# Optimization experiments

Measured on AMD Instinct MI355X. Metric: run time of the kernel, lower is better.

## Reference

```python
import jax, jax.numpy as jnp
import numpy as np

B, C, H, W = 16, 128, 64, 64
L, ND = 512, 256
GROUPS = 32
EPS = 1e-6


def setup_inputs() -> dict:
    key = jax.random.key(0)
    ks = jax.random.split(key, 8)
    return {
        "x": jax.random.normal(ks[0], (B, C, H, W), dtype=jnp.float32),
        "nd": jax.random.normal(ks[1], (B, L, ND), dtype=jnp.float32),
        "gn_gamma": jnp.ones((C,), dtype=jnp.float32),
        "gn_beta": jnp.zeros((C,), dtype=jnp.float32),
        "q_w": jax.random.normal(ks[2], (C, C), dtype=jnp.float32) * 0.02,
        "q_b": jax.random.normal(ks[3], (C,), dtype=jnp.float32) * 0.02,
        "nd_w": jax.random.normal(ks[4], (C, ND), dtype=jnp.float32) * 0.02,
        "nd_b": jax.random.normal(ks[5], (C,), dtype=jnp.float32) * 0.02,
        "proj_w": jax.random.normal(ks[6], (C, C), dtype=jnp.float32) * 0.02,
        "proj_b": jax.random.normal(ks[7], (C,), dtype=jnp.float32) * 0.02,
    }


def _group_norm(x, gamma, beta):
    b, c, h, w = x.shape
    xr = x.reshape(b, GROUPS, c // GROUPS, h, w)
    mean = xr.mean(axis=(2, 3, 4), keepdims=True)
    var = xr.var(axis=(2, 3, 4), keepdims=True)
    xn = ((xr - mean) * jax.lax.rsqrt(var + EPS)).reshape(b, c, h, w)
    return xn * gamma[None, :, None, None] + beta[None, :, None, None]


def reference(x, nd, gn_gamma, gn_beta, q_w, q_b, nd_w, nd_b, proj_w, proj_b):
    b, c, h, w = x.shape
    hn = _group_norm(x, gn_gamma, gn_beta)
    # 1x1 conv query -> [b, hw, c]
    q = jnp.einsum('bchw,oc->bhwo', hn, q_w).reshape(b, h * w, c) + q_b
    # silu + linear projection of conditioning; k and v use identical projection/input
    kv = jax.nn.silu(nd) @ nd_w.T + nd_b  # [b, L, c]
    # attention: [b, hw, L]
    logits = jnp.einsum('bnc,blc->bnl', q, kv) * (c ** -0.5)
    attn = jax.nn.softmax(logits, axis=2)
    # weighted sum of v -> [b, c, hw] -> [b, c, h, w]
    out = jnp.einsum('blc,bnl->bcn', kv, attn).reshape(b, c, h, w)
    # 1x1 conv projection
    out = jnp.einsum('bchw,oc->bohw', out, proj_w) + proj_b[None, :, None, None]
    return x + out
```

## Files before the change

kernel.cpp:

```cpp
#include <hip/hip_runtime.h>
#include <math.h>

constexpr int kB = 16, kC = 128, kHW = 4096, kL = 512, kND = 256, kG = 32;
constexpr float kEps = 1e-6f;
constexpr float kScale = 0.08838834764831845f;

typedef short sv8 __attribute__((ext_vector_type(8)));
typedef int   iv4 __attribute__((ext_vector_type(4)));
typedef float f32x16 __attribute__((ext_vector_type(16)));

static __device__ __forceinline__ unsigned short f2bf(float f) {
    unsigned int u = __builtin_bit_cast(unsigned int, f);
    u += 0x7fffu + ((u >> 16) & 1u);
    return (unsigned short)(u >> 16);
}
static __device__ __forceinline__ float bf2f(unsigned short s) {
    unsigned int u = ((unsigned int)s) << 16;
    return __builtin_bit_cast(float, u);
}
static __device__ __forceinline__ unsigned int pack2(float a, float b) {
    return (unsigned int)f2bf(a) | ((unsigned int)f2bf(b) << 16);
}

#define GLOAD_LDS16(gp, lp)                                                     \
    __builtin_amdgcn_global_load_lds(                                           \
        (const __attribute__((address_space(1))) void*)(gp),                    \
        (__attribute__((address_space(3))) void*)(lp), 16, 0, 0)

__global__ __launch_bounds__(256) void prep_all_k(
    const float* __restrict__ x, const float* __restrict__ nd,
    const float* __restrict__ nd_w, const float* __restrict__ nd_b,
    const float* __restrict__ proj_w,
    float* __restrict__ stats, unsigned short* __restrict__ kv_bf,
    unsigned short* __restrict__ kvT_bf, unsigned short* __restrict__ pwb)
{
    __shared__ float s_lds[8][256];
    __shared__ float w_lds[128][68];
    __shared__ float t_lds[8][129];
    __shared__ float red8[8];
    const int bid = blockIdx.x;
    const int tid = threadIdx.x;

    if (bid < 512) {
        const float4* p4 = (const float4*)(x + (size_t)bid * 4 * kHW);
        float s = 0.f, ss = 0.f;
        for (int i = tid; i < 4096; i += 256) {
            float4 v = p4[i];
            s  += (v.x + v.y) + (v.z + v.w);
            ss += (v.x * v.x + v.y * v.y) + (v.z * v.z + v.w * v.w);
        }
#pragma unroll
        for (int off = 1; off < 64; off <<= 1) {
            s  += __shfl_xor(s, off, 64);
            ss += __shfl_xor(ss, off, 64);
        }
        int wid = tid >> 6;
        if ((tid & 63) == 0) { red8[wid] = s; red8[wid + 4] = ss; }
        __syncthreads();
        if (tid == 0) {
            float S  = (red8[0] + red8[1]) + (red8[2] + red8[3]);
            float SS = (red8[4] + red8[5]) + (red8[6] + red8[7]);
            float mean = S * (1.f / 16384.f);
            float var  = SS * (1.f / 16384.f) - mean * mean;
            stats[bid * 2]     = mean;
            stats[bid * 2 + 1] = rsqrtf(var + kEps);
        }
        return;
    }
    if (bid >= 1536) {
        int i = ((bid - 1536) * 256 + tid) * 4;
        float4 v = *(const float4*)(proj_w + i);
        pwb[i + 0] = f2bf(v.x); pwb[i + 1] = f2bf(v.y);
        pwb[i + 2] = f2bf(v.z); pwb[i + 3] = f2bf(v.w);
        return;
    }
    {
        int idx0 = bid - 512;
        int b = idx0 >> 6;
        int l0 = (idx0 & 63) * 8;
        const float4* ndp = (const float4*)(nd + ((size_t)b * kL + l0) * kND);
#pragma unroll
        for (int r = 0; r < 2; r++) {
            int idx = tid + r * 256;
            int row = idx >> 6;
            int c4 = idx & 63;
            float4 v = ndp[row * 64 + c4];
            v.x = v.x / (1.f + __expf(-v.x));
            v.y = v.y / (1.f + __expf(-v.y));
            v.z = v.z / (1.f + __expf(-v.z));
            v.w = v.w / (1.f + __expf(-v.w));
            *(float4*)&s_lds[row][c4 * 4] = v;
        }
        float acc[4] = {0.f, 0.f, 0.f, 0.f};
        int lr = tid >> 5;
        int oq = tid & 31;
        for (int d0 = 0; d0 < kND; d0 += 64) {
            __syncthreads();
#pragma unroll
            for (int r = 0; r < 8; r++) {
                int idx = tid + r * 256;
                int row = idx >> 4;
                int c4 = idx & 15;
                float4 v = ((const float4*)(nd_w + (size_t)row * kND + d0))[c4];
                *(float4*)&w_lds[row][c4 * 4] = v;
            }
            __syncthreads();
            for (int dd = 0; dd < 64; dd += 4) {
                float4 sv = *(const float4*)&s_lds[lr][d0 + dd];
#pragma unroll
                for (int j = 0; j < 4; j++) {
                    float4 wv = *(const float4*)&w_lds[oq + 32 * j][dd];
                    acc[j] += sv.x * wv.x + sv.y * wv.y + sv.z * wv.z + sv.w * wv.w;
                }
            }
        }
#pragma unroll
        for (int j = 0; j < 4; j++) {
            int o = oq + 32 * j;
            float vout = acc[j] + nd_b[o];
            kv_bf[((size_t)b * kL + l0 + lr) * kC + o] = f2bf(vout);
            t_lds[lr][o] = vout;
        }
        __syncthreads();
        int o = tid >> 1, lh = (tid & 1) * 4;
        unsigned long long pk = 0;
#pragma unroll
        for (int i = 0; i < 4; i++)
            pk |= (unsigned long long)f2bf(t_lds[lh + i][o]) << (16 * i);
        *(unsigned long long*)(kvT_bf + ((size_t)b * kC + o) * kL + l0 + lh) = pk;
    }
}

__global__ __launch_bounds__(256, 2) void attn_k(
    const float* __restrict__ x,
    const float* __restrict__ stats,
    const float* __restrict__ gamma,
    const float* __restrict__ beta,
    const float* __restrict__ q_w,
    const float* __restrict__ q_b,
    const unsigned short* __restrict__ kvb,
    const unsigned short* __restrict__ kvtb,
    const unsigned short* __restrict__ pwb,
    const float* __restrict__ proj_b,
    float* __restrict__ out)
{
    __shared__ __align__(16) char smem[36864];

    const int flat = blockIdx.y * gridDim.x + blockIdx.x;
    const int b  = ((flat & 7) << 1) | ((flat >> 3) & 1);
    const int n0 = (flat >> 4) * 128;
    const int tid = threadIdx.x;
    const int wave = tid >> 6;
    const int lane = tid & 63;
    const int lrow = lane & 31;
    const int hi = lane >> 5;
    const int swzA = (lrow & 15) << 4;
    const int swzT = ((lrow >> 1) & 3) << 4;

    unsigned short* qw = (unsigned short*)smem;
    float* gtab = (float*)(smem + 34816);

    if (tid < 128) {
        float mean = stats[(b * kG + (tid >> 2)) * 2];
        float rstd = stats[(b * kG + (tid >> 2)) * 2 + 1];
        float ga = gamma[tid] * rstd;
        gtab[tid] = ga;
        gtab[128 + tid] = beta[tid] - mean * ga;
        gtab[256 + tid] = q_b[tid];
    }
#pragma unroll
    for (int r = 0; r < 16; r++) {
        int idx = tid + r * 256;
        int row = idx >> 5, c4 = idx & 31;
        float4 v = ((const float4*)q_w)[idx];
        unsigned int lo = (unsigned int)f2bf(v.x) | ((unsigned int)f2bf(v.y) << 16);
        unsigned int h2 = (unsigned int)f2bf(v.z) | ((unsigned int)f2bf(v.w) << 16);
        *(uint2*)&qw[row * 136 + c4 * 4] = make_uint2(lo, h2);
    }
    __syncthreads();

    sv8 hn[8];
    {
        const float* xp = x + (size_t)b * kC * kHW + n0 + wave * 32 + lrow;
#pragma unroll
        for (int kc = 0; kc < 8; kc++) {
            int cb = kc * 16 + hi * 8;
            sv8 a;
#pragma unroll
            for (int j = 0; j < 8; j++) {
                float ga = gtab[cb + j], be = gtab[128 + cb + j];
                a[j] = (short)f2bf(xp[(size_t)(cb + j) * kHW] * ga + be);
            }
            hn[kc] = a;
        }
    }
    f32x16 dq[4];
#pragma unroll
    for (int ot = 0; ot < 4; ot++)
#pragma unroll
        for (int r = 0; r < 16; r++) dq[ot][r] = 0.f;
#pragma unroll
    for (int ot = 0; ot < 4; ot++) {
        const unsigned short* arow = qw + (ot * 32 + lrow) * 136 + hi * 8;
#pragma unroll
        for (int kc = 0; kc < 8; kc++)
            dq[ot] = __builtin_amdgcn_mfma_f32_32x32x16_bf16(
                         *(const sv8*)(arow + kc * 16), hn[kc], dq[ot], 0, 0, 0);
    }
    sv8 qa[8];
#pragma unroll
    for (int ot = 0; ot < 4; ot++) {
        unsigned int pk[4], pk2[4];
#pragma unroll
        for (int g = 0; g < 4; g++) {
            int ob = ot * 32 + 8 * g + 4 * hi;
            float v0 = (dq[ot][4 * g + 0] + gtab[256 + ob + 0]) * kScale;
            float v1 = (dq[ot][4 * g + 1] + gtab[256 + ob + 1]) * kScale;
            float v2 = (dq[ot][4 * g + 2] + gtab[256 + ob + 2]) * kScale;
            float v3 = (dq[ot][4 * g + 3] + gtab[256 + ob + 3]) * kScale;
            pk[g]  = pack2(v0, v1);
            pk2[g] = pack2(v2, v3);
        }
#pragma unroll
        for (int kk = 0; kk < 2; kk++) {
            unsigned int a_lo = pk[kk * 2],  a_hi = pk[kk * 2 + 1];
            unsigned int b_lo = pk2[kk * 2], b_hi = pk2[kk * 2 + 1];
            unsigned int own_a = hi ? a_hi : a_lo;
            unsigned int own_b = hi ? b_hi : b_lo;
            unsigned int rcv_a = (unsigned int)__shfl_xor((int)(hi ? a_lo : a_hi), 32, 64);
            unsigned int rcv_b = (unsigned int)__shfl_xor((int)(hi ? b_lo : b_hi), 32, 64);
            iv4 w;
            w[0] = (int)(hi ? rcv_a : own_a);
            w[1] = (int)(hi ? rcv_b : own_b);
            w[2] = (int)(hi ? own_a : rcv_a);
            w[3] = (int)(hi ? own_b : rcv_b);
            qa[2 * ot + kk] = __builtin_bit_cast(sv8, w);
        }
    }
    __syncthreads();

    f32x16 oacc[4];
#pragma unroll
    for (int ct = 0; ct < 4; ct++)
#pragma unroll
        for (int r = 0; r < 16; r++) oacc[ct][r] = 0.f;
    float rsumv = 0.f;

    const unsigned short* kvB  = kvb  + (size_t)b * kL * kC;
    const unsigned short* kvtB = kvtb + (size_t)b * kC * kL;

#define STAGE_TILE(tt) do {                                                     \
        int l0s = (tt) << 5;                                                    \
        char* dA = smem + (((tt) & 1) * 8192);                                  \
        char* dT = smem + 16384 + (((tt) & 1) * 8192);                          \
        _Pragma("unroll")                                                       \
        for (int i = 0; i < 2; i++) {                                           \
            int l = i * 16 + wave * 4 + (lane >> 4);                            \
            int ch = lane & 15;                                                 \
            const unsigned short* gs =                                          \
                kvB + (size_t)(l0s + l) * kC + ((ch ^ (l & 15)) * 8);           \
            GLOAD_LDS16(gs, dA + (i * 256 + wave * 64) * 16);                   \
        }                                                                       \
        _Pragma("unroll")                                                       \
        for (int i = 0; i < 2; i++) {                                           \
            int c = i * 64 + wave * 16 + (lane >> 2);                           \
            int ch = lane & 3;                                                  \
            const unsigned short* gs =                                          \
                kvtB + (size_t)c * kL + l0s + ((ch ^ ((c >> 1) & 3)) * 8);      \
            GLOAD_LDS16(gs, dT + (i * 256 + wave * 64) * 16);                   \
        }                                                                       \
    } while (0)

    STAGE_TILE(0);
    __syncthreads();

    for (int t = 0; t < 16; t++) {
        const char* bufA = smem + (t & 1) * 8192;
        const char* bufT = smem + 16384 + (t & 1) * 8192;
        if (t < 15) STAGE_TILE(t + 1);

        f32x16 s;
#pragma unroll
        for (int r = 0; r < 16; r++) s[r] = 0.f;
        {
            const char* arow = bufA + lrow * 256;
            __builtin_amdgcn_s_setprio(1);
#pragma unroll
            for (int kc = 0; kc < 8; kc++)
                s = __builtin_amdgcn_mfma_f32_32x32x16_bf16(
                        *(const sv8*)(arow + ((kc * 32 + hi * 16) ^ swzA)),
                        qa[kc], s, 0, 0, 0);
            __builtin_amdgcn_s_setprio(0);
        }
        float p[16];
#pragma unroll
        for (int r = 0; r < 16; r++) {
            p[r] = __expf(s[r]);
            rsumv += p[r];
        }
        unsigned int pk[4], pk2[4];
#pragma unroll
        for (int g = 0; g < 4; g++) {
            pk[g]  = pack2(p[4 * g + 0], p[4 * g + 1]);
            pk2[g] = pack2(p[4 * g + 2], p[4 * g + 3]);
        }
        sv8 pv[2];
#pragma unroll
        for (int kk = 0; kk < 2; kk++) {
            unsigned int a_lo = pk[kk * 2],  a_hi = pk[kk * 2 + 1];
            unsigned int b_lo = pk2[kk * 2], b_hi = pk2[kk * 2 + 1];
            unsigned int own_a = hi ? a_hi : a_lo;
            unsigned int own_b = hi ? b_hi : b_lo;
            unsigned int rcv_a = (unsigned int)__shfl_xor((int)(hi ? a_lo : a_hi), 32, 64);
            unsigned int rcv_b = (unsigned int)__shfl_xor((int)(hi ? b_lo : b_hi), 32, 64);
            iv4 w;
            w[0] = (int)(hi ? rcv_a : own_a);
            w[1] = (int)(hi ? rcv_b : own_b);
            w[2] = (int)(hi ? own_a : rcv_a);
            w[3] = (int)(hi ? own_b : rcv_b);
            pv[kk] = __builtin_bit_cast(sv8, w);
        }
        __builtin_amdgcn_s_setprio(1);
#pragma unroll
        for (int ct = 0; ct < 4; ct++) {
            const char* rowp = bufT + (ct * 32 + lrow) * 64;
#pragma unroll
            for (int kk = 0; kk < 2; kk++)
                oacc[ct] = __builtin_amdgcn_mfma_f32_32x32x16_bf16(
                               pv[kk],
                               *(const sv8*)(rowp + ((kk * 32 + hi * 16) ^ swzT)),
                               oacc[ct], 0, 0, 0);
        }
        __builtin_amdgcn_s_setprio(0);

        __syncthreads();
    }

    float total = rsumv + __shfl_xor(rsumv, 32, 64);
    float* rs = (float*)(smem + 36352) + wave * 32;
    rs[lrow] = 1.0f / total;
    float rinv[16];
#pragma unroll
    for (int r = 0; r < 16; r++)
        rinv[r] = rs[(r & 3) + 8 * (r >> 2) + 4 * hi];

    unsigned short* o_lds = (unsigned short*)smem;
    __syncthreads();
#pragma unroll
    for (int ct = 0; ct < 4; ct++)
#pragma unroll
        for (int r = 0; r < 16; r++) {
            int n = wave * 32 + (r & 3) + 8 * (r >> 2) + 4 * hi;
            o_lds[n * 136 + ct * 32 + lrow] = f2bf(oacc[ct][r] * rinv[r]);
        }
    sv8 oa[8];
    {
        const unsigned short* orow = o_lds + (wave * 32 + lrow) * 136 + hi * 8;
#pragma unroll
        for (int kc = 0; kc < 8; kc++) oa[kc] = *(const sv8*)(orow + kc * 16);
    }
    f32x16 dacc[4];
#pragma unroll
    for (int ot = 0; ot < 4; ot++)
#pragma unroll
        for (int r = 0; r < 16; r++) dacc[ot][r] = 0.f;
#pragma unroll
    for (int ot = 0; ot < 4; ot++) {
        const unsigned short* brow = pwb + (ot * 32 + lrow) * kC + hi * 8;
#pragma unroll
        for (int kc = 0; kc < 8; kc++)
            dacc[ot] = __builtin_amdgcn_mfma_f32_32x32x16_bf16(
                           oa[kc], *(const sv8*)(brow + kc * 16), dacc[ot], 0, 0, 0);
    }
#pragma unroll
    for (int ot = 0; ot < 4; ot++)
#pragma unroll
        for (int r = 0; r < 16; r++) {
            int n = wave * 32 + (r & 3) + 8 * (r >> 2) + 4 * hi;
            o_lds[n * 136 + ot * 32 + lrow] = f2bf(dacc[ot][r]);
        }
    __syncthreads();
#pragma unroll 4
    for (int it = 0; it < 64; it++) {
        int idx = it * 256 + tid;
        int o = idx >> 7, n = idx & 127;
        size_t gi = ((size_t)b * kC + o) * kHW + n0 + n;
        out[gi] = bf2f(o_lds[n * 136 + o]) + proj_b[o] + x[gi];
    }
#undef STAGE_TILE
}

extern "C" void kernel_launch(void* const* d_in, const int* in_sizes, int n_in,
                              void* d_out, int out_size, void* d_ws, size_t ws_size,
                              hipStream_t stream) {
    const float* x      = (const float*)d_in[0];
    const float* nd     = (const float*)d_in[1];
    const float* gamma  = (const float*)d_in[2];
    const float* beta   = (const float*)d_in[3];
    const float* q_w    = (const float*)d_in[4];
    const float* q_b    = (const float*)d_in[5];
    const float* nd_w   = (const float*)d_in[6];
    const float* nd_b   = (const float*)d_in[7];
    const float* proj_w = (const float*)d_in[8];
    const float* proj_b = (const float*)d_in[9];
    float* out = (float*)d_out;

    float* stats           = (float*)d_ws;
    unsigned short* pwb    = (unsigned short*)(stats + 1024);
    unsigned short* kv_bf  = pwb + 16384;
    unsigned short* kvT_bf = kv_bf + (size_t)kB * kL * kC;

    prep_all_k<<<dim3(1552), dim3(256), 0, stream>>>(
        x, nd, nd_w, nd_b, proj_w, stats, kv_bf, kvT_bf, pwb);
    attn_k<<<dim3(kHW / 128, kB), dim3(256), 0, stream>>>(
        x, stats, gamma, beta, q_w, q_b, kv_bf, kvT_bf, pwb, proj_b, out);
}
```

Baseline: 81.16 us.

## Overlap first KV tile staging with query projection prologue

Issues the first K/V tile async load before the query-projection prologue, so the staging overlaps the GroupNorm and Q GEMM work. The prologue is restructured: all 64 x values are loaded into registers up front, and the q_w weight is staged in two halves through a separate LDS region so the attention buffers stay untouched. LDS grows from 36 KB to 51 KB per block, which may still allow two blocks per CU. The trade-offs are higher register pressure from 64 extra live floats and an added barrier.

```diff
diff --git a/kernel.cpp b/kernel.cpp
--- a/kernel.cpp
+++ b/kernel.cpp
@@ -144,7 +144,7 @@
     const float* __restrict__ proj_b,
     float* __restrict__ out)
 {
-    __shared__ __align__(16) char smem[36864];
+    __shared__ __align__(16) char smem[52224];
 
     const int flat = blockIdx.y * gridDim.x + blockIdx.x;
     const int b  = ((flat & 7) << 1) | ((flat >> 3) & 1);
@@ -157,94 +157,8 @@
     const int swzA = (lrow & 15) << 4;
     const int swzT = ((lrow >> 1) & 3) << 4;
 
-    unsigned short* qw = (unsigned short*)smem;
-    float* gtab = (float*)(smem + 34816);
-
-    if (tid < 128) {
-        float mean = stats[(b * kG + (tid >> 2)) * 2];
-        float rstd = stats[(b * kG + (tid >> 2)) * 2 + 1];
-        float ga = gamma[tid] * rstd;
-        gtab[tid] = ga;
-        gtab[128 + tid] = beta[tid] - mean * ga;
-        gtab[256 + tid] = q_b[tid];
-    }
-#pragma unroll
-    for (int r = 0; r < 16; r++) {
-        int idx = tid + r * 256;
-        int row = idx >> 5, c4 = idx & 31;
-        float4 v = ((const float4*)q_w)[idx];
-        unsigned int lo = (unsigned int)f2bf(v.x) | ((unsigned int)f2bf(v.y) << 16);
-        unsigned int h2 = (unsigned int)f2bf(v.z) | ((unsigned int)f2bf(v.w) << 16);
-        *(uint2*)&qw[row * 136 + c4 * 4] = make_uint2(lo, h2);
-    }
-    __syncthreads();
-
-    sv8 hn[8];
-    {
-        const float* xp = x + (size_t)b * kC * kHW + n0 + wave * 32 + lrow;
-#pragma unroll
-        for (int kc = 0; kc < 8; kc++) {
-            int cb = kc * 16 + hi * 8;
-            sv8 a;
-#pragma unroll
-            for (int j = 0; j < 8; j++) {
-                float ga = gtab[cb + j], be = gtab[128 + cb + j];
-                a[j] = (short)f2bf(xp[(size_t)(cb + j) * kHW] * ga + be);
-            }
-            hn[kc] = a;
-        }
-    }
-    f32x16 dq[4];
-#pragma unroll
-    for (int ot = 0; ot < 4; ot++)
-#pragma unroll
-        for (int r = 0; r < 16; r++) dq[ot][r] = 0.f;
-#pragma unroll
-    for (int ot = 0; ot < 4; ot++) {
-        const unsigned short* arow = qw + (ot * 32 + lrow) * 136 + hi * 8;
-#pragma unroll
-        for (int kc = 0; kc < 8; kc++)
-            dq[ot] = __builtin_amdgcn_mfma_f32_32x32x16_bf16(
-                         *(const sv8*)(arow + kc * 16), hn[kc], dq[ot], 0, 0, 0);
-    }
-    sv8 qa[8];
-#pragma unroll
-    for (int ot = 0; ot < 4; ot++) {
-        unsigned int pk[4], pk2[4];
-#pragma unroll
-        for (int g = 0; g < 4; g++) {
-            int ob = ot * 32 + 8 * g + 4 * hi;
-            float v0 = (dq[ot][4 * g + 0] + gtab[256 + ob + 0]) * kScale;
-            float v1 = (dq[ot][4 * g + 1] + gtab[256 + ob + 1]) * kScale;
-            float v2 = (dq[ot][4 * g + 2] + gtab[256 + ob + 2]) * kScale;
-            float v3 = (dq[ot][4 * g + 3] + gtab[256 + ob + 3]) * kScale;
-            pk[g]  = pack2(v0, v1);
-            pk2[g] = pack2(v2, v3);
-        }
-#pragma unroll
-        for (int kk = 0; kk < 2; kk++) {
-            unsigned int a_lo = pk[kk * 2],  a_hi = pk[kk * 2 + 1];
-            unsigned int b_lo = pk2[kk * 2], b_hi = pk2[kk * 2 + 1];
-            unsigned int own_a = hi ? a_hi : a_lo;
-            unsigned int own_b = hi ? b_hi : b_lo;
-            unsigned int rcv_a = (unsigned int)__shfl_xor((int)(hi ? a_lo : a_hi), 32, 64);
-            unsigned int rcv_b = (unsigned int)__shfl_xor((int)(hi ? b_lo : b_hi), 32, 64);
-            iv4 w;
-            w[0] = (int)(hi ? rcv_a : own_a);
-            w[1] = (int)(hi ? rcv_b : own_b);
-            w[2] = (int)(hi ? own_a : rcv_a);
-            w[3] = (int)(hi ? own_b : rcv_b);
-            qa[2 * ot + kk] = __builtin_bit_cast(sv8, w);
-        }
-    }
-    __syncthreads();
-
-    f32x16 oacc[4];
-#pragma unroll
-    for (int ct = 0; ct < 4; ct++)
-#pragma unroll
-        for (int r = 0; r < 16; r++) oacc[ct][r] = 0.f;
-    float rsumv = 0.f;
+    unsigned short* qw = (unsigned short*)(smem + 32768);
+    float* gtab = (float*)(smem + 50176);
 
     const unsigned short* kvB  = kvb  + (size_t)b * kL * kC;
     const unsigned short* kvtB = kvtb + (size_t)b * kC * kL;
@@ -272,7 +186,130 @@
     } while (0)
 
     STAGE_TILE(0);
+
+    if (tid < 128) {
+        float mean = stats[(b * kG + (tid >> 2)) * 2];
+        float rstd = stats[(b * kG + (tid >> 2)) * 2 + 1];
+        float ga = gamma[tid] * rstd;
+        gtab[tid] = ga;
+        gtab[128 + tid] = beta[tid] - mean * ga;
+        gtab[256 + tid] = q_b[tid];
+    }
+    float xv[64];
+    {
+        const float* xp = x + (size_t)b * kC * kHW + n0 + wave * 32 + lrow;
+#pragma unroll
+        for (int c = 0; c < 64; c++) {
+            int ch = (c >> 3) * 16 + hi * 8 + (c & 7);
+            xv[c] = xp[(size_t)ch * kHW];
+        }
+    }
+#pragma unroll
+    for (int r = 0; r < 8; r++) {
+        int idx = tid + r * 256;
+        int row = idx >> 5, c4 = idx & 31;
+        float4 v = ((const float4*)q_w)[row * 32 + c4];
+        unsigned int lo = (unsigned int)f2bf(v.x) | ((unsigned int)f2bf(v.y) << 16);
+        unsigned int h2 = (unsigned int)f2bf(v.z) | ((unsigned int)f2bf(v.w) << 16);
+        *(uint2*)&qw[row * 136 + c4 * 4] = make_uint2(lo, h2);
+    }
     __syncthreads();
+
+    float4 cv[8];
+#pragma unroll
+    for (int r = 0; r < 8; r++) {
+        int idx = tid + r * 256;
+        int row = idx >> 5, c4 = idx & 31;
+        cv[r] = ((const float4*)q_w)[(64 + row) * 32 + c4];
+    }
+    sv8 hn[8];
+#pragma unroll
+    for (int kc = 0; kc < 8; kc++) {
+        int cb = kc * 16 + hi * 8;
+        float4 g0 = *(const float4*)&gtab[cb];
+        float4 g1 = *(const float4*)&gtab[cb + 4];
+        float4 e0 = *(const float4*)&gtab[128 + cb];
+        float4 e1 = *(const float4*)&gtab[128 + cb + 4];
+        sv8 a;
+        a[0] = (short)f2bf(xv[kc * 8 + 0] * g0.x + e0.x);
+        a[1] = (short)f2bf(xv[kc * 8 + 1] * g0.y + e0.y);
+        a[2] = (short)f2bf(xv[kc * 8 + 2] * g0.z + e0.z);
+        a[3] = (short)f2bf(xv[kc * 8 + 3] * g0.w + e0.w);
+        a[4] = (short)f2bf(xv[kc * 8 + 4] * g1.x + e1.x);
+        a[5] = (short)f2bf(xv[kc * 8 + 5] * g1.y + e1.y);
+        a[6] = (short)f2bf(xv[kc * 8 + 6] * g1.z + e1.z);
+        a[7] = (short)f2bf(xv[kc * 8 + 7] * g1.w + e1.w);
+        hn[kc] = a;
+    }
+    f32x16 dq[4];
+#pragma unroll
+    for (int ot = 0; ot < 4; ot++)
+#pragma unroll
+        for (int r = 0; r < 16; r++) dq[ot][r] = 0.f;
+#pragma unroll
+    for (int ot = 0; ot < 2; ot++) {
+        const unsigned short* arow = qw + (ot * 32 + lrow) * 136 + hi * 8;
+#pragma unroll
+        for (int kc = 0; kc < 8; kc++)
+            dq[ot] = __builtin_amdgcn_mfma_f32_32x32x16_bf16(
+                         *(const sv8*)(arow + kc * 16), hn[kc], dq[ot], 0, 0, 0);
+    }
+    __syncthreads();
+#pragma unroll
+    for (int r = 0; r < 8; r++) {
+        int idx = tid + r * 256;
+        int row = idx >> 5, c4 = idx & 31;
+        float4 v = cv[r];
+        unsigned int lo = (unsigned int)f2bf(v.x) | ((unsigned int)f2bf(v.y) << 16);
+        unsigned int h2 = (unsigned int)f2bf(v.z) | ((unsigned int)f2bf(v.w) << 16);
+        *(uint2*)&qw[row * 136 + c4 * 4] = make_uint2(lo, h2);
+    }
+    __syncthreads();
+#pragma unroll
+    for (int ot = 2; ot < 4; ot++) {
+        const unsigned short* arow = qw + ((ot - 2) * 32 + lrow) * 136 + hi * 8;
+#pragma unroll
+        for (int kc = 0; kc < 8; kc++)
+            dq[ot] = __builtin_amdgcn_mfma_f32_32x32x16_bf16(
+                         *(const sv8*)(arow + kc * 16), hn[kc], dq[ot], 0, 0, 0);
+    }
+    sv8 qa[8];
+#pragma unroll
+    for (int ot = 0; ot < 4; ot++) {
+        unsigned int pk[4], pk2[4];
+#pragma unroll
+        for (int g = 0; g < 4; g++) {
+            int ob = ot * 32 + 8 * g + 4 * hi;
+            float v0 = (dq[ot][4 * g + 0] + gtab[256 + ob + 0]) * kScale;
+            float v1 = (dq[ot][4 * g + 1] + gtab[256 + ob + 1]) * kScale;
+            float v2 = (dq[ot][4 * g + 2] + gtab[256 + ob + 2]) * kScale;
+            float v3 = (dq[ot][4 * g + 3] + gtab[256 + ob + 3]) * kScale;
+            pk[g]  = pack2(v0, v1);
+            pk2[g] = pack2(v2, v3);
+        }
+#pragma unroll
+        for (int kk = 0; kk < 2; kk++) {
+            unsigned int a_lo = pk[kk * 2],  a_hi = pk[kk * 2 + 1];
+            unsigned int b_lo = pk2[kk * 2], b_hi = pk2[kk * 2 + 1];
+            unsigned int own_a = hi ? a_hi : a_lo;
+            unsigned int own_b = hi ? b_hi : b_lo;
+            unsigned int rcv_a = (unsigned int)__shfl_xor((int)(hi ? a_lo : a_hi), 32, 64);
+            unsigned int rcv_b = (unsigned int)__shfl_xor((int)(hi ? b_lo : b_hi), 32, 64);
+            iv4 w;
+            w[0] = (int)(hi ? rcv_a : own_a);
+            w[1] = (int)(hi ? rcv_b : own_b);
+            w[2] = (int)(hi ? own_a : rcv_a);
+            w[3] = (int)(hi ? own_b : rcv_b);
+            qa[2 * ot + kk] = __builtin_bit_cast(sv8, w);
+        }
+    }
+
+    f32x16 oacc[4];
+#pragma unroll
+    for (int ct = 0; ct < 4; ct++)
+#pragma unroll
+        for (int r = 0; r < 16; r++) oacc[ct][r] = 0.f;
+    float rsumv = 0.f;
 
     for (int t = 0; t < 16; t++) {
         const char* bufA = smem + (t & 1) * 8192;
@@ -337,7 +374,7 @@
     }
 
     float total = rsumv + __shfl_xor(rsumv, 32, 64);
-    float* rs = (float*)(smem + 36352) + wave * 32;
+    float* rs = (float*)(smem + 51712) + wave * 32;
     rs[lrow] = 1.0f / total;
     float rinv[16];
 #pragma unroll
```

After: 80.62 us. About the same (-0.7%).

## Split query projection into separate kernel writing bf16 Q to workspace

Applied to the files above, without the earlier changes.

Moves the GroupNorm-apply and 1x1 query convolution out of the attention kernel into a new qproj_k kernel. That kernel stages x and bf16 weights in swizzled LDS with coalesced float4 loads and writes scaled bf16 Q to workspace. The attention kernel then just loads its Q fragments directly, which replaces the strided per-channel x reads and shuffles and cuts its LDS use. The cost is an extra kernel launch plus a write and re-read of Q (16x4096x128 bf16) through global memory.

```diff
diff --git a/kernel.cpp b/kernel.cpp
--- a/kernel.cpp
+++ b/kernel.cpp
@@ -131,20 +131,111 @@
     }
 }
 
+__global__ __launch_bounds__(256) void qproj_k(
+    const float* __restrict__ x, const float* __restrict__ stats,
+    const float* __restrict__ gamma, const float* __restrict__ beta,
+    const float* __restrict__ q_w, const float* __restrict__ q_b,
+    unsigned short* __restrict__ q_bf)
+{
+    __shared__ __align__(16) char smem[44032];
+    const int b = blockIdx.y;
+    const int n0 = blockIdx.x * 128;
+    const int tid = threadIdx.x;
+    const int wave = tid >> 6, lane = tid & 63;
+    const int lrow = lane & 31, hi = lane >> 5;
+
+    unsigned short* hn = (unsigned short*)(smem + 32768);
+    float* gab = (float*)(smem + 43008);
+
+    if (tid < 128) {
+        float mean = stats[(b * kG + (tid >> 2)) * 2];
+        float rstd = stats[(b * kG + (tid >> 2)) * 2 + 1];
+        float ga = gamma[tid] * rstd;
+        gab[tid] = ga;
+        gab[128 + tid] = beta[tid] - mean * ga;
+    }
+#pragma unroll
+    for (int k = 0; k < 8; k++) {
+        int idx = tid + k * 256;
+        int o = idx >> 4, ch = idx & 15;
+        float4 v0 = ((const float4*)q_w)[o * 32 + ch * 2];
+        float4 v1 = ((const float4*)q_w)[o * 32 + ch * 2 + 1];
+        uint4 pk;
+        pk.x = pack2(v0.x, v0.y); pk.y = pack2(v0.z, v0.w);
+        pk.z = pack2(v1.x, v1.y); pk.w = pack2(v1.z, v1.w);
+        *(uint4*)(smem + o * 256 + ((ch ^ (o & 15)) * 16)) = pk;
+    }
+    __syncthreads();
+
+    f32x16 dq[4];
+#pragma unroll
+    for (int ot = 0; ot < 4; ot++)
+#pragma unroll
+        for (int r = 0; r < 16; r++) dq[ot][r] = 0.f;
+
+    for (int cc = 0; cc < 4; cc++) {
+#pragma unroll
+        for (int k = 0; k < 4; k++) {
+            int idx = tid + k * 256;
+            int c = idx >> 5, n4 = idx & 31;
+            float4 v = *(const float4*)(
+                x + ((size_t)b * kC + cc * 32 + c) * kHW + n0 + n4 * 4);
+            float ga = gab[cc * 32 + c], be = gab[128 + cc * 32 + c];
+            hn[(n4 * 4 + 0) * 40 + c] = f2bf(v.x * ga + be);
+            hn[(n4 * 4 + 1) * 40 + c] = f2bf(v.y * ga + be);
+            hn[(n4 * 4 + 2) * 40 + c] = f2bf(v.z * ga + be);
+            hn[(n4 * 4 + 3) * 40 + c] = f2bf(v.w * ga + be);
+        }
+        __syncthreads();
+        sv8 fa[2];
+#pragma unroll
+        for (int kk = 0; kk < 2; kk++)
+            fa[kk] = *(const sv8*)(hn + (wave * 32 + lrow) * 40 + kk * 16 + hi * 8);
+#pragma unroll
+        for (int ot = 0; ot < 4; ot++) {
+            int o = ot * 32 + lrow;
+#pragma unroll
+            for (int kk = 0; kk < 2; kk++) {
+                const sv8* bq = (const sv8*)(smem + o * 256 +
+                    (((cc * 4 + kk * 2 + hi) ^ (o & 15)) * 16));
+                dq[ot] = __builtin_amdgcn_mfma_f32_32x32x16_bf16(
+                             fa[kk], *bq, dq[ot], 0, 0, 0);
+            }
+        }
+        __syncthreads();
+    }
+
+    unsigned short* q_out = (unsigned short*)smem;
+#pragma unroll
+    for (int ot = 0; ot < 4; ot++) {
+        int o = ot * 32 + lrow;
+        float qb = q_b[o];
+#pragma unroll
+        for (int r = 0; r < 16; r++) {
+            int n_loc = wave * 32 + (r & 3) + 8 * (r >> 2) + 4 * hi;
+            q_out[n_loc * 136 + o] = f2bf((dq[ot][r] + qb) * kScale);
+        }
+    }
+    __syncthreads();
+#pragma unroll
+    for (int r = 0; r < 8; r++) {
+        int idx = tid + r * 256;
+        int n = idx >> 4, ch = idx & 15;
+        *(uint4*)(q_bf + ((size_t)b * kHW + n0 + n) * kC + ch * 8) =
+            *(const uint4*)&q_out[n * 136 + ch * 8];
+    }
+}
+
 __global__ __launch_bounds__(256, 2) void attn_k(
-    const float* __restrict__ x,
-    const float* __restrict__ stats,
-    const float* __restrict__ gamma,
-    const float* __restrict__ beta,
-    const float* __restrict__ q_w,
-    const float* __restrict__ q_b,
+    const unsigned short* __restrict__ qb,
     const unsigned short* __restrict__ kvb,
     const unsigned short* __restrict__ kvtb,
     const unsigned short* __restrict__ pwb,
     const float* __restrict__ proj_b,
+    const float* __restrict__ x,
     float* __restrict__ out)
 {
-    __shared__ __align__(16) char smem[36864];
+    __shared__ __align__(16) char smem[35328];
 
     const int flat = blockIdx.y * gridDim.x + blockIdx.x;
     const int b  = ((flat & 7) << 1) | ((flat >> 3) & 1);
@@ -157,87 +248,14 @@
     const int swzA = (lrow & 15) << 4;
     const int swzT = ((lrow >> 1) & 3) << 4;
 
-    unsigned short* qw = (unsigned short*)smem;
-    float* gtab = (float*)(smem + 34816);
-
-    if (tid < 128) {
-        float mean = stats[(b * kG + (tid >> 2)) * 2];
-        float rstd = stats[(b * kG + (tid >> 2)) * 2 + 1];
-        float ga = gamma[tid] * rstd;
-        gtab[tid] = ga;
-        gtab[128 + tid] = beta[tid] - mean * ga;
-        gtab[256 + tid] = q_b[tid];
-    }
-#pragma unroll
-    for (int r = 0; r < 16; r++) {
-        int idx = tid + r * 256;
-        int row = idx >> 5, c4 = idx & 31;
-        float4 v = ((const float4*)q_w)[idx];
-        unsigned int lo = (unsigned int)f2bf(v.x) | ((unsigned int)f2bf(v.y) << 16);
-        unsigned int h2 = (unsigned int)f2bf(v.z) | ((unsigned int)f2bf(v.w) << 16);
-        *(uint2*)&qw[row * 136 + c4 * 4] = make_uint2(lo, h2);
-    }
-    __syncthreads();
-
-    sv8 hn[8];
+    sv8 qa[8];
     {
-        const float* xp = x + (size_t)b * kC * kHW + n0 + wave * 32 + lrow;
-#pragma unroll
-        for (int kc = 0; kc < 8; kc++) {
-            int cb = kc * 16 + hi * 8;
-            sv8 a;
-#pragma unroll
-            for (int j = 0; j < 8; j++) {
-                float ga = gtab[cb + j], be = gtab[128 + cb + j];
-                a[j] = (short)f2bf(xp[(size_t)(cb + j) * kHW] * ga + be);
-            }
-            hn[kc] = a;
-        }
-    }
-    f32x16 dq[4];
-#pragma unroll
-    for (int ot = 0; ot < 4; ot++)
-#pragma unroll
-        for (int r = 0; r < 16; r++) dq[ot][r] = 0.f;
-#pragma unroll
-    for (int ot = 0; ot < 4; ot++) {
-        const unsigned short* arow = qw + (ot * 32 + lrow) * 136 + hi * 8;
+        const unsigned short* qrow =
+            qb + ((size_t)b * kHW + n0 + wave * 32 + lrow) * kC + hi * 8;
 #pragma unroll
         for (int kc = 0; kc < 8; kc++)
-            dq[ot] = __builtin_amdgcn_mfma_f32_32x32x16_bf16(
-                         *(const sv8*)(arow + kc * 16), hn[kc], dq[ot], 0, 0, 0);
-    }
-    sv8 qa[8];
-#pragma unroll
-    for (int ot = 0; ot < 4; ot++) {
-        unsigned int pk[4], pk2[4];
-#pragma unroll
-        for (int g = 0; g < 4; g++) {
-            int ob = ot * 32 + 8 * g + 4 * hi;
-            float v0 = (dq[ot][4 * g + 0] + gtab[256 + ob + 0]) * kScale;
-            float v1 = (dq[ot][4 * g + 1] + gtab[256 + ob + 1]) * kScale;
-            float v2 = (dq[ot][4 * g + 2] + gtab[256 + ob + 2]) * kScale;
-            float v3 = (dq[ot][4 * g + 3] + gtab[256 + ob + 3]) * kScale;
-            pk[g]  = pack2(v0, v1);
-            pk2[g] = pack2(v2, v3);
-        }
-#pragma unroll
-        for (int kk = 0; kk < 2; kk++) {
-            unsigned int a_lo = pk[kk * 2],  a_hi = pk[kk * 2 + 1];
-            unsigned int b_lo = pk2[kk * 2], b_hi = pk2[kk * 2 + 1];
-            unsigned int own_a = hi ? a_hi : a_lo;
-            unsigned int own_b = hi ? b_hi : b_lo;
-            unsigned int rcv_a = (unsigned int)__shfl_xor((int)(hi ? a_lo : a_hi), 32, 64);
-            unsigned int rcv_b = (unsigned int)__shfl_xor((int)(hi ? b_lo : b_hi), 32, 64);
-            iv4 w;
-            w[0] = (int)(hi ? rcv_a : own_a);
-            w[1] = (int)(hi ? rcv_b : own_b);
-            w[2] = (int)(hi ? own_a : rcv_a);
-            w[3] = (int)(hi ? own_b : rcv_b);
-            qa[2 * ot + kk] = __builtin_bit_cast(sv8, w);
-        }
-    }
-    __syncthreads();
+            qa[kc] = *(const sv8*)(qrow + kc * 16);
+    }
 
     f32x16 oacc[4];
 #pragma unroll
@@ -337,7 +355,7 @@
     }
 
     float total = rsumv + __shfl_xor(rsumv, 32, 64);
-    float* rs = (float*)(smem + 36352) + wave * 32;
+    float* rs = (float*)(smem + 34816) + wave * 32;
     rs[lrow] = 1.0f / total;
     float rinv[16];
 #pragma unroll
@@ -409,9 +427,12 @@
     unsigned short* pwb    = (unsigned short*)(stats + 1024);
     unsigned short* kv_bf  = pwb + 16384;
     unsigned short* kvT_bf = kv_bf + (size_t)kB * kL * kC;
+    unsigned short* q_bf   = kvT_bf + (size_t)kB * kL * kC;
 
     prep_all_k<<<dim3(1552), dim3(256), 0, stream>>>(
         x, nd, nd_w, nd_b, proj_w, stats, kv_bf, kvT_bf, pwb);
+    qproj_k<<<dim3(kHW / 128, kB), dim3(256), 0, stream>>>(
+        x, stats, gamma, beta, q_w, q_b, q_bf);
     attn_k<<<dim3(kHW / 128, kB), dim3(256), 0, stream>>>(
-        x, stats, gamma, beta, q_w, q_b, kv_bf, kvT_bf, pwb, proj_b, out);
-}
+        q_bf, kv_bf, kvT_bf, pwb, proj_b, x, out);
+}
```

After: 91.55 us. 1.13x slower.

## Halve attention block size, precompute bf16 q_w, stage group-norm input through LDS

Applied to the files above, without the earlier changes.

The attention kernel now runs 128-thread blocks that each cover 64 spatial positions, so twice as many blocks are launched. The q_w bf16 conversion moves into the prep kernel instead of being repeated by every attention block. The group-norm input is read with coalesced float4 loads into LDS in 32-channel chunks, and the first KV tile prefetch is issued before the query projection. More blocks per batch means the K/V tiles are streamed from memory more times in total, and the chunked query GEMM adds extra barriers.

```diff
diff --git a/kernel.cpp b/kernel.cpp
--- a/kernel.cpp
+++ b/kernel.cpp
@@ -30,9 +30,10 @@
 __global__ __launch_bounds__(256) void prep_all_k(
     const float* __restrict__ x, const float* __restrict__ nd,
     const float* __restrict__ nd_w, const float* __restrict__ nd_b,
-    const float* __restrict__ proj_w,
+    const float* __restrict__ proj_w, const float* __restrict__ q_w,
     float* __restrict__ stats, unsigned short* __restrict__ kv_bf,
-    unsigned short* __restrict__ kvT_bf, unsigned short* __restrict__ pwb)
+    unsigned short* __restrict__ kvT_bf, unsigned short* __restrict__ pwb,
+    unsigned short* __restrict__ qwb)
 {
     __shared__ float s_lds[8][256];
     __shared__ float w_lds[128][68];
@@ -68,10 +69,12 @@
         return;
     }
     if (bid >= 1536) {
-        int i = ((bid - 1536) * 256 + tid) * 4;
-        float4 v = *(const float4*)(proj_w + i);
-        pwb[i + 0] = f2bf(v.x); pwb[i + 1] = f2bf(v.y);
-        pwb[i + 2] = f2bf(v.z); pwb[i + 3] = f2bf(v.w);
+        const float* src = (bid < 1552) ? proj_w : q_w;
+        unsigned short* dst = (bid < 1552) ? pwb : qwb;
+        int i = (((bid - 1536) & 15) * 256 + tid) * 4;
+        float4 v = *(const float4*)(src + i);
+        dst[i + 0] = f2bf(v.x); dst[i + 1] = f2bf(v.y);
+        dst[i + 2] = f2bf(v.z); dst[i + 3] = f2bf(v.w);
         return;
     }
     {
@@ -131,12 +134,12 @@
     }
 }
 
-__global__ __launch_bounds__(256, 2) void attn_k(
+__global__ __launch_bounds__(128, 2) void attn_k(
     const float* __restrict__ x,
     const float* __restrict__ stats,
     const float* __restrict__ gamma,
     const float* __restrict__ beta,
-    const float* __restrict__ q_w,
+    const unsigned short* __restrict__ qwb,
     const float* __restrict__ q_b,
     const unsigned short* __restrict__ kvb,
     const unsigned short* __restrict__ kvtb,
@@ -144,11 +147,11 @@
     const float* __restrict__ proj_b,
     float* __restrict__ out)
 {
-    __shared__ __align__(16) char smem[36864];
+    __shared__ __align__(16) char smem[33024];
 
     const int flat = blockIdx.y * gridDim.x + blockIdx.x;
     const int b  = ((flat & 7) << 1) | ((flat >> 3) & 1);
-    const int n0 = (flat >> 4) * 128;
+    const int n0 = (flat >> 4) * 64;
     const int tid = threadIdx.x;
     const int wave = tid >> 6;
     const int lane = tid & 63;
@@ -157,55 +160,76 @@
     const int swzA = (lrow & 15) << 4;
     const int swzT = ((lrow >> 1) & 3) << 4;
 
-    unsigned short* qw = (unsigned short*)smem;
-    float* gtab = (float*)(smem + 34816);
-
-    if (tid < 128) {
-        float mean = stats[(b * kG + (tid >> 2)) * 2];
-        float rstd = stats[(b * kG + (tid >> 2)) * 2 + 1];
-        float ga = gamma[tid] * rstd;
-        gtab[tid] = ga;
-        gtab[128 + tid] = beta[tid] - mean * ga;
-        gtab[256 + tid] = q_b[tid];
-    }
-#pragma unroll
-    for (int r = 0; r < 16; r++) {
-        int idx = tid + r * 256;
-        int row = idx >> 5, c4 = idx & 31;
-        float4 v = ((const float4*)q_w)[idx];
-        unsigned int lo = (unsigned int)f2bf(v.x) | ((unsigned int)f2bf(v.y) << 16);
-        unsigned int h2 = (unsigned int)f2bf(v.z) | ((unsigned int)f2bf(v.w) << 16);
-        *(uint2*)&qw[row * 136 + c4 * 4] = make_uint2(lo, h2);
-    }
-    __syncthreads();
-
-    sv8 hn[8];
-    {
-        const float* xp = x + (size_t)b * kC * kHW + n0 + wave * 32 + lrow;
-#pragma unroll
-        for (int kc = 0; kc < 8; kc++) {
-            int cb = kc * 16 + hi * 8;
+    const unsigned short* kvB  = kvb  + (size_t)b * kL * kC;
+    const unsigned short* kvtB = kvtb + (size_t)b * kC * kL;
+
+#define STAGE_TILE(tt) do {                                                     \
+        int l0s = (tt) << 5;                                                    \
+        char* dA = smem + (((tt) & 1) * 8192);                                  \
+        char* dT = smem + 16384 + (((tt) & 1) * 8192);                          \
+        _Pragma("unroll")                                                       \
+        for (int i = 0; i < 4; i++) {                                           \
+            int idx = i * 128 + wave * 64 + lane;                               \
+            int l = idx >> 4, ch = idx & 15;                                    \
+            const unsigned short* gs =                                          \
+                kvB + (size_t)(l0s + l) * kC + ((ch ^ (l & 15)) * 8);           \
+            GLOAD_LDS16(gs, dA + (i * 128 + wave * 64) * 16);                   \
+        }                                                                       \
+        _Pragma("unroll")                                                       \
+        for (int i = 0; i < 4; i++) {                                           \
+            int idx = i * 128 + wave * 64 + lane;                               \
+            int c = idx >> 2, ch = idx & 3;                                     \
+            const unsigned short* gs =                                          \
+                kvtB + (size_t)c * kL + l0s + ((ch ^ ((c >> 1) & 3)) * 8);      \
+            GLOAD_LDS16(gs, dT + (i * 128 + wave * 64) * 16);                   \
+        }                                                                       \
+    } while (0)
+
+    STAGE_TILE(0);
+
+    float* hn_f = (float*)(smem + 8192);
+    f32x16 dq[4];
+#pragma unroll
+    for (int ot = 0; ot < 4; ot++)
+#pragma unroll
+        for (int r = 0; r < 16; r++) dq[ot][r] = 0.f;
+
+    for (int cc = 0; cc < 4; cc++) {
+#pragma unroll
+        for (int k = 0; k < 4; k++) {
+            int cl = k * 8 + (tid >> 4);
+            int c = cc * 32 + cl;
+            int n4 = tid & 15;
+            float4 v = *(const float4*)(
+                x + ((size_t)b * kC + c) * kHW + n0 + n4 * 4);
+            float mean = stats[(b * kG + (c >> 2)) * 2];
+            float rstd = stats[(b * kG + (c >> 2)) * 2 + 1];
+            float ga = gamma[c] * rstd;
+            float be = beta[c] - mean * ga;
+            v.x = v.x * ga + be; v.y = v.y * ga + be;
+            v.z = v.z * ga + be; v.w = v.w * ga + be;
+            *(float4*)&hn_f[cl * 64 + n4 * 4] = v;
+        }
+        __syncthreads();
+        sv8 bh[2];
+#pragma unroll
+        for (int kk = 0; kk < 2; kk++) {
             sv8 a;
 #pragma unroll
-            for (int j = 0; j < 8; j++) {
-                float ga = gtab[cb + j], be = gtab[128 + cb + j];
-                a[j] = (short)f2bf(xp[(size_t)(cb + j) * kHW] * ga + be);
-            }
-            hn[kc] = a;
-        }
-    }
-    f32x16 dq[4];
-#pragma unroll
-    for (int ot = 0; ot < 4; ot++)
-#pragma unroll
-        for (int r = 0; r < 16; r++) dq[ot][r] = 0.f;
-#pragma unroll
-    for (int ot = 0; ot < 4; ot++) {
-        const unsigned short* arow = qw + (ot * 32 + lrow) * 136 + hi * 8;
-#pragma unroll
-        for (int kc = 0; kc < 8; kc++)
-            dq[ot] = __builtin_amdgcn_mfma_f32_32x32x16_bf16(
-                         *(const sv8*)(arow + kc * 16), hn[kc], dq[ot], 0, 0, 0);
+            for (int j = 0; j < 8; j++)
+                a[j] = (short)f2bf(hn_f[(kk * 16 + hi * 8 + j) * 64 + wave * 32 + lrow]);
+            bh[kk] = a;
+        }
+#pragma unroll
+        for (int ot = 0; ot < 4; ot++) {
+            const unsigned short* arow =
+                qwb + (size_t)(ot * 32 + lrow) * kC + cc * 32 + hi * 8;
+#pragma unroll
+            for (int kk = 0; kk < 2; kk++)
+                dq[ot] = __builtin_amdgcn_mfma_f32_32x32x16_bf16(
+                             *(const sv8*)(arow + kk * 16), bh[kk], dq[ot], 0, 0, 0);
+        }
+        __syncthreads();
     }
     sv8 qa[8];
 #pragma unroll
@@ -214,10 +238,11 @@
 #pragma unroll
         for (int g = 0; g < 4; g++) {
             int ob = ot * 32 + 8 * g + 4 * hi;
-            float v0 = (dq[ot][4 * g + 0] + gtab[256 + ob + 0]) * kScale;
-            float v1 = (dq[ot][4 * g + 1] + gtab[256 + ob + 1]) * kScale;
-            float v2 = (dq[ot][4 * g + 2] + gtab[256 + ob + 2]) * kScale;
-            float v3 = (dq[ot][4 * g + 3] + gtab[256 + ob + 3]) * kScale;
+            float4 qb4 = *(const float4*)(q_b + ob);
+            float v0 = (dq[ot][4 * g + 0] + qb4.x) * kScale;
+            float v1 = (dq[ot][4 * g + 1] + qb4.y) * kScale;
+            float v2 = (dq[ot][4 * g + 2] + qb4.z) * kScale;
+            float v3 = (dq[ot][4 * g + 3] + qb4.w) * kScale;
             pk[g]  = pack2(v0, v1);
             pk2[g] = pack2(v2, v3);
         }
@@ -237,7 +262,6 @@
             qa[2 * ot + kk] = __builtin_bit_cast(sv8, w);
         }
     }
-    __syncthreads();
 
     f32x16 oacc[4];
 #pragma unroll
@@ -245,34 +269,6 @@
 #pragma unroll
         for (int r = 0; r < 16; r++) oacc[ct][r] = 0.f;
     float rsumv = 0.f;
-
-    const unsigned short* kvB  = kvb  + (size_t)b * kL * kC;
-    const unsigned short* kvtB = kvtb + (size_t)b * kC * kL;
-
-#define STAGE_TILE(tt) do {                                                     \
-        int l0s = (tt) << 5;                                                    \
-        char* dA = smem + (((tt) & 1) * 8192);                                  \
-        char* dT = smem + 16384 + (((tt) & 1) * 8192);                          \
-        _Pragma("unroll")                                                       \
-        for (int i = 0; i < 2; i++) {                                           \
-            int l = i * 16 + wave * 4 + (lane >> 4);                            \
-            int ch = lane & 15;                                                 \
-            const unsigned short* gs =                                          \
-                kvB + (size_t)(l0s + l) * kC + ((ch ^ (l & 15)) * 8);           \
-            GLOAD_LDS16(gs, dA + (i * 256 + wave * 64) * 16);                   \
-        }                                                                       \
-        _Pragma("unroll")                                                       \
-        for (int i = 0; i < 2; i++) {                                           \
-            int c = i * 64 + wave * 16 + (lane >> 2);                           \
-            int ch = lane & 3;                                                  \
-            const unsigned short* gs =                                          \
-                kvtB + (size_t)c * kL + l0s + ((ch ^ ((c >> 1) & 3)) * 8);      \
-            GLOAD_LDS16(gs, dT + (i * 256 + wave * 64) * 16);                   \
-        }                                                                       \
-    } while (0)
-
-    STAGE_TILE(0);
-    __syncthreads();
 
     for (int t = 0; t < 16; t++) {
         const char* bufA = smem + (t & 1) * 8192;
@@ -337,7 +333,7 @@
     }
 
     float total = rsumv + __shfl_xor(rsumv, 32, 64);
-    float* rs = (float*)(smem + 36352) + wave * 32;
+    float* rs = (float*)(smem + 32768) + wave * 32;
     rs[lrow] = 1.0f / total;
     float rinv[16];
 #pragma unroll
@@ -382,8 +378,8 @@
     __syncthreads();
 #pragma unroll 4
     for (int it = 0; it < 64; it++) {
-        int idx = it * 256 + tid;
-        int o = idx >> 7, n = idx & 127;
+        int idx = it * 128 + tid;
+        int o = idx >> 6, n = idx & 63;
         size_t gi = ((size_t)b * kC + o) * kHW + n0 + n;
         out[gi] = bf2f(o_lds[n * 136 + o]) + proj_b[o] + x[gi];
     }
@@ -407,11 +403,12 @@
 
     float* stats           = (float*)d_ws;
     unsigned short* pwb    = (unsigned short*)(stats + 1024);
-    unsigned short* kv_bf  = pwb + 16384;
+    unsigned short* qwb    = pwb + 16384;
+    unsigned short* kv_bf  = qwb + 16384;
     unsigned short* kvT_bf = kv_bf + (size_t)kB * kL * kC;
 
-    prep_all_k<<<dim3(1552), dim3(256), 0, stream>>>(
-        x, nd, nd_w, nd_b, proj_w, stats, kv_bf, kvT_bf, pwb);
-    attn_k<<<dim3(kHW / 128, kB), dim3(256), 0, stream>>>(
-        x, stats, gamma, beta, q_w, q_b, kv_bf, kvT_bf, pwb, proj_b, out);
-}
+    prep_all_k<<<dim3(1568), dim3(256), 0, stream>>>(
+        x, nd, nd_w, nd_b, proj_w, q_w, stats, kv_bf, kvT_bf, pwb, qwb);
+    attn_k<<<dim3(kHW / 64, kB), dim3(128), 0, stream>>>(
+        x, stats, gamma, beta, qwb, q_b, kv_bf, kvT_bf, pwb, proj_b, out);
+}
```

New measurement: 87.84 us. +8.2%, slower.
